# Kernel tuning notes

Measured on AMD Instinct MI355X. Metric: run time of the kernel, lower is better.

The kernel has to match this reference:

```python
import jax, jax.numpy as jnp
import numpy as np

LABEL_SMOOTH = 0.1

def setup_inputs() -> dict:
    key = jax.random.key(0)
    k1, k2, k3, k4 = jax.random.split(key, 4)
    B, S, D, V = 2, 2048, 1024, 50257
    targets = jax.random.randint(k1, (B, S), 0, V)              # int labels in [0, V)
    masks = jax.random.randint(k2, (B, S), 0, 2).astype(bool)   # valid-token mask
    outputs = jax.random.normal(k3, (B, S, D), dtype=jnp.float32)
    W = jax.random.normal(k4, (V, D), dtype=jnp.float32) * 0.02  # nn.Linear(d_model, V, bias=False).weight
    return {"targets": targets, "masks": masks, "outputs": outputs, "W": W}

def reference(targets, masks, outputs, W):
    # Faithful to IO.cost: gather masked tokens, project to vocab, label-smoothed NLL.
    # Boolean gather is expressed as mask-weighted means (identical math, jit-friendly).
    V = W.shape[0]
    logits = jnp.einsum('bsd,vd->bsv', outputs, W)        # [B,S,V] huge intermediate
    logp = jax.nn.log_softmax(logits, axis=-1)            # [B,S,V]
    m = masks.astype(logp.dtype)                          # [B,S]
    n_valid = m.sum()
    # F.nll_loss(logits, targets): mean of -logp[target] over valid tokens
    tok_logp = jnp.take_along_axis(logp, targets[..., None], axis=-1)[..., 0]  # [B,S]
    nll = -(m * tok_logp).sum() / n_valid
    # logits.mean(): mean of log-probs over valid tokens x vocab
    mean_logp = (m * logp.sum(axis=-1)).sum() / (n_valid * V)
    return nll * (1.0 - LABEL_SMOOTH) - mean_logp * LABEL_SMOOTH
```

## Files before the change

kernel.cpp:

```cpp
#include <hip/hip_runtime.h>
#include <hip/hip_bf16.h>
#include <stdint.h>

#define T_TOK 4096
#define DIM   1024
#define VOC   50257
#define VPAD  51200
#define BK    128
#define NKS   8

#define FRAGB  2048
#define PANB   16384

#define WSCALE 64.0f
#define INV_WSCALE 0.015625f

typedef __attribute__((ext_vector_type(8))) int  i32x8;
typedef __attribute__((ext_vector_type(4))) float f32x4;

__device__ __forceinline__ uint32_t pk4_fp8(float a, float b, float c, float d) {
  int u = 0;
  u = __builtin_amdgcn_cvt_pk_fp8_f32(a, b, u, false);
  u = __builtin_amdgcn_cvt_pk_fp8_f32(c, d, u, true);
  return (uint32_t)u;
}

__device__ __forceinline__ i32x8 ld32(const uint8_t* p) {
  const int4 lo = *(const int4*)p;
  const int4 hi = *(const int4*)(p + 16);
  i32x8 r;
  r[0] = lo.x; r[1] = lo.y; r[2] = lo.z; r[3] = lo.w;
  r[4] = hi.x; r[5] = hi.y; r[6] = hi.z; r[7] = hi.w;
  return r;
}

__global__ void k_scan(const int* __restrict__ masks, const int* __restrict__ targets,
                       int* __restrict__ hdr, int* __restrict__ cidx, int* __restrict__ tgtc,
                       float* __restrict__ Se, float* __restrict__ Sl) {
  __shared__ int cnt[256];
  const int tid = threadIdx.x;
  const int base = tid * 16;
  #pragma unroll
  for (int i = 0; i < 16; i++) { Se[base + i] = 0.f; Sl[base + i] = 0.f; }
  int c = 0;
  #pragma unroll
  for (int i = 0; i < 16; i++) c += (masks[base + i] != 0) ? 1 : 0;
  cnt[tid] = c;
  __syncthreads();
  for (int off = 1; off < 256; off <<= 1) {
    int add = (tid >= off) ? cnt[tid - off] : 0;
    __syncthreads();
    cnt[tid] += add;
    __syncthreads();
  }
  int start = cnt[tid] - c;
  for (int i = 0; i < 16; i++) {
    int t = base + i;
    if (masks[t] != 0) { cidx[start] = t; tgtc[start] = targets[t]; start++; }
  }
  if (tid == 255) hdr[0] = cnt[255];
}

__global__ void k_xconv(const float* __restrict__ X, const int* __restrict__ hdr,
                        const int* __restrict__ cidx, uint8_t* __restrict__ XqT) {
  const int c4 = blockIdx.x * 256 + threadIdx.x;
  const int slot = c4 >> 8;
  const int kq   = c4 & 255;
  const int p = slot >> 4, rlo = slot & 15;
  const int s = kq >> 5;
  const int w128 = kq & 31;
  const int q = w128 >> 3;
  const int b = (w128 & 7) * 4;
  const int l = q * 16 + rlo;
  const int nv = hdr[0];
  uint32_t o = 0;
  if (slot < nv) {
    const float4 v = *(const float4*)(X + (size_t)cidx[slot] * DIM + (size_t)kq * 4);
    o = pk4_fp8(v.x, v.y, v.z, v.w);
  }
  *(uint32_t*)(XqT + (size_t)(p * 8 + s) * 2048 + l * 32 + b) = o;
}

__global__ void k_wconv(const float* __restrict__ W, uint8_t* __restrict__ WqT) {
  const int c4 = blockIdx.x * 256 + threadIdx.x;
  const int row = c4 >> 8;
  const int kq  = c4 & 255;
  const int p = row >> 4, rlo = row & 15;
  const int s = kq >> 5;
  const int w128 = kq & 31;
  const int q = w128 >> 3;
  const int b = (w128 & 7) * 4;
  const int l = q * 16 + rlo;
  uint32_t o = 0;
  if (row < VOC) {
    const float4 v = *(const float4*)(W + (size_t)row * DIM + (size_t)kq * 4);
    o = pk4_fp8(v.x * WSCALE, v.y * WSCALE, v.z * WSCALE, v.w * WSCALE);
  }
  *(uint32_t*)(WqT + (size_t)(p * 8 + s) * 2048 + l * 32 + b) = o;
}

__global__ __launch_bounds__(256) void k_gemm(
    const uint8_t* __restrict__ XqT, const uint8_t* __restrict__ WqT,
    const int* __restrict__ hdr, const int* __restrict__ tgtc,
    float* __restrict__ tlog, float* __restrict__ Se, float* __restrict__ Sl) {
  const int flat = blockIdx.x;
  const int xcd = flat & 7;
  const int u = flat >> 3;
  const int ms = u & 63;
  const int ng = (u >> 6) * 8 + xcd;

  const int nv = hdr[0];
  const int m0 = ms * 64;
  if (m0 >= nv) return;

  const int tid = threadIdx.x;
  const int w    = tid >> 6;
  const int lane = tid & 63;
  const int quad = lane >> 4;
  const int l15  = lane & 15;
  const int n0w  = (ng * 4 + w) * 64;

  const uint8_t* pA[4];
  const uint8_t* pB[4];
  #pragma unroll
  for (int i = 0; i < 4; i++) {
    pA[i] = XqT + (size_t)(ms * 4 + i) * PANB + lane * 32;
    pB[i] = WqT + (size_t)((n0w >> 4) + i) * PANB + lane * 32;
  }

  f32x4 acc[4][4];
  #pragma unroll
  for (int i = 0; i < 4; i++)
    #pragma unroll
    for (int j = 0; j < 4; j++) { f32x4 z = {0.f, 0.f, 0.f, 0.f}; acc[i][j] = z; }

  const int sc1 = 0x7F7F7F7F;

  i32x8 a0[4], b0[4], a1[4], b1[4];
  #pragma unroll
  for (int i = 0; i < 4; i++) { a0[i] = ld32(pA[i]); b0[i] = ld32(pB[i]); }

  #pragma unroll
  for (int s = 0; s < NKS; s += 2) {
    if (s + 1 < NKS) {
      #pragma unroll
      for (int i = 0; i < 4; i++) {
        a1[i] = ld32(pA[i] + (s + 1) * FRAGB);
        b1[i] = ld32(pB[i] + (s + 1) * FRAGB);
      }
    }
    #pragma unroll
    for (int mi = 0; mi < 4; mi++)
      #pragma unroll
      for (int ni = 0; ni < 4; ni++)
        acc[mi][ni] = __builtin_amdgcn_mfma_scale_f32_16x16x128_f8f6f4(
            a0[mi], b0[ni], acc[mi][ni], 0, 0, 0, sc1, 0, sc1);
    if (s + 2 < NKS) {
      #pragma unroll
      for (int i = 0; i < 4; i++) {
        a0[i] = ld32(pA[i] + (s + 2) * FRAGB);
        b0[i] = ld32(pB[i] + (s + 2) * FRAGB);
      }
    }
    if (s + 1 < NKS) {
      #pragma unroll
      for (int mi = 0; mi < 4; mi++)
        #pragma unroll
        for (int ni = 0; ni < 4; ni++)
          acc[mi][ni] = __builtin_amdgcn_mfma_scale_f32_16x16x128_f8f6f4(
              a1[mi], b1[ni], acc[mi][ni], 0, 0, 0, sc1, 0, sc1);
    }
  }

  int tg[4][4];
  #pragma unroll
  for (int mi = 0; mi < 4; mi++) {
    const int4 t4 = *(const int4*)&tgtc[m0 + mi * 16 + quad * 4];
    tg[mi][0] = t4.x; tg[mi][1] = t4.y; tg[mi][2] = t4.z; tg[mi][3] = t4.w;
  }
  float rse[4][4], rsl[4][4];
  #pragma unroll
  for (int mi = 0; mi < 4; mi++)
    #pragma unroll
    for (int r = 0; r < 4; r++) { rse[mi][r] = 0.f; rsl[mi][r] = 0.f; }
  #pragma unroll
  for (int ni = 0; ni < 4; ni++) {
    const int v = n0w + ni * 16 + l15;
    if (v < VOC) {
      #pragma unroll
      for (int mi = 0; mi < 4; mi++)
        #pragma unroll
        for (int r = 0; r < 4; r++) {
          const float x = acc[mi][ni][r] * INV_WSCALE;
          rse[mi][r] += __expf(x);
          rsl[mi][r] += x;
          if (v == tg[mi][r]) tlog[m0 + mi * 16 + quad * 4 + r] = x;
        }
    }
  }
  #pragma unroll
  for (int off = 1; off < 16; off <<= 1)
    #pragma unroll
    for (int mi = 0; mi < 4; mi++)
      #pragma unroll
      for (int r = 0; r < 4; r++) {
        rse[mi][r] += __shfl_xor(rse[mi][r], off, 16);
        rsl[mi][r] += __shfl_xor(rsl[mi][r], off, 16);
      }

  __shared__ float seP[4][64], slP[4][64];
  if (l15 == 0) {
    #pragma unroll
    for (int mi = 0; mi < 4; mi++)
      #pragma unroll
      for (int r = 0; r < 4; r++) {
        const int row = mi * 16 + quad * 4 + r;
        seP[w][row] = rse[mi][r];
        slP[w][row] = rsl[mi][r];
      }
  }
  __syncthreads();
  if (tid < 64) {
    const int t = m0 + tid;
    if (t < nv) {
      atomicAdd(&Se[t], seP[0][tid] + seP[1][tid] + seP[2][tid] + seP[3][tid]);
      atomicAdd(&Sl[t], slP[0][tid] + slP[1][tid] + slP[2][tid] + slP[3][tid]);
    }
  }
}

__global__ void k_final(const int* __restrict__ hdr, const float* __restrict__ Se,
                        const float* __restrict__ Sl, const float* __restrict__ tlog,
                        float* __restrict__ out) {
  __shared__ float rn[256], rs[256];
  const int tid = threadIdx.x;
  const int nv = hdr[0];
  float nll = 0.f, slg = 0.f;
  for (int t = tid; t < nv; t += 256) {
    const float lse = logf(Se[t]);
    nll += lse - tlog[t];
    slg += Sl[t] - (float)VOC * lse;
  }
  rn[tid] = nll; rs[tid] = slg;
  __syncthreads();
  for (int off = 128; off > 0; off >>= 1) {
    if (tid < off) { rn[tid] += rn[tid + off]; rs[tid] += rs[tid + off]; }
    __syncthreads();
  }
  if (tid == 0) {
    const float fnv = (float)nv;
    out[0] = 0.9f * (rn[0] / fnv) - 0.1f * (rs[0] / (fnv * (float)VOC));
  }
}

extern "C" void kernel_launch(void* const* d_in, const int* in_sizes, int n_in,
                              void* d_out, int out_size, void* d_ws, size_t ws_size,
                              hipStream_t stream) {
  const int*   targets = (const int*)d_in[0];
  const int*   masks   = (const int*)d_in[1];
  const float* X       = (const float*)d_in[2];
  const float* W       = (const float*)d_in[3];

  uint8_t* ws = (uint8_t*)d_ws;
  size_t off = 0;
  auto alloc = [&](size_t n) { size_t p = off; off += (n + 255) & ~(size_t)255; return p; };
  int*      hdr  = (int*)     (ws + alloc(256));
  int*      cidx = (int*)     (ws + alloc((size_t)T_TOK * 4));
  int*      tgtc = (int*)     (ws + alloc((size_t)T_TOK * 4));
  float*    tlog = (float*)   (ws + alloc((size_t)T_TOK * 4));
  float*    Se   = (float*)   (ws + alloc((size_t)T_TOK * 4));
  float*    Sl   = (float*)   (ws + alloc((size_t)T_TOK * 4));
  uint8_t*  XqT  = (uint8_t*) (ws + alloc((size_t)T_TOK * DIM));
  uint8_t*  WqT  = (uint8_t*) (ws + alloc((size_t)VPAD * DIM));

  k_scan<<<dim3(1), dim3(256), 0, stream>>>(masks, targets, hdr, cidx, tgtc, Se, Sl);
  k_xconv<<<dim3(T_TOK * DIM / 4 / 256), dim3(256), 0, stream>>>(X, hdr, cidx, XqT);
  k_wconv<<<dim3(VPAD * DIM / 4 / 256), dim3(256), 0, stream>>>(W, WqT);
  k_gemm<<<dim3(64 * 200), dim3(256), 0, stream>>>(XqT, WqT, hdr, tgtc, tlog, Se, Sl);
  k_final<<<dim3(1), dim3(256), 0, stream>>>(hdr, Se, Sl, tlog, (float*)d_out);
}
```

Before: 591.6 us.

## Fuse W fp8 conversion into GEMM with LDS-resident vocab slice per block

Removes the separate W quantization kernel and its global round trip. Each GEMM block now loads a 64-row slice of W, converts it to fp8 into shared memory once, keeps the B fragments in registers, and loops over all token tiles streaming A from global. This cuts the 200MB fp32 W read plus fp8 write and re-read down to a single read. The cost is that only 786 blocks, each with a 64KB LDS tile, perform a serial loop over token tiles with syncs. Per-block compute is also reduced to 4 MFMAs per k-step, which may lower MFMA utilization and increase A-operand traffic.

```diff
diff --git a/kernel.cpp b/kernel.cpp
--- a/kernel.cpp
+++ b/kernel.cpp
@@ -5,8 +5,7 @@
 #define T_TOK 4096
 #define DIM   1024
 #define VOC   50257
-#define VPAD  51200
-#define BK    128
+#define NBLK  786
 #define NKS   8
 
 #define FRAGB  2048
@@ -81,151 +80,146 @@
   *(uint32_t*)(XqT + (size_t)(p * 8 + s) * 2048 + l * 32 + b) = o;
 }
 
-__global__ void k_wconv(const float* __restrict__ W, uint8_t* __restrict__ WqT) {
-  const int c4 = blockIdx.x * 256 + threadIdx.x;
-  const int row = c4 >> 8;
-  const int kq  = c4 & 255;
-  const int p = row >> 4, rlo = row & 15;
-  const int s = kq >> 5;
-  const int w128 = kq & 31;
-  const int q = w128 >> 3;
-  const int b = (w128 & 7) * 4;
-  const int l = q * 16 + rlo;
-  uint32_t o = 0;
-  if (row < VOC) {
-    const float4 v = *(const float4*)(W + (size_t)row * DIM + (size_t)kq * 4);
-    o = pk4_fp8(v.x * WSCALE, v.y * WSCALE, v.z * WSCALE, v.w * WSCALE);
-  }
-  *(uint32_t*)(WqT + (size_t)(p * 8 + s) * 2048 + l * 32 + b) = o;
-}
-
-__global__ __launch_bounds__(256) void k_gemm(
-    const uint8_t* __restrict__ XqT, const uint8_t* __restrict__ WqT,
+__global__ __launch_bounds__(256, 2) void k_gemm(
+    const uint8_t* __restrict__ XqT, const float* __restrict__ W,
     const int* __restrict__ hdr, const int* __restrict__ tgtc,
     float* __restrict__ tlog, float* __restrict__ Se, float* __restrict__ Sl) {
-  const int flat = blockIdx.x;
-  const int xcd = flat & 7;
-  const int u = flat >> 3;
-  const int ms = u & 63;
-  const int ng = (u >> 6) * 8 + xcd;
-
-  const int nv = hdr[0];
-  const int m0 = ms * 64;
-  if (m0 >= nv) return;
-
+  __shared__ __align__(16) uint8_t Blds[65536];
+  __shared__ float seP[4][64], slP[4][64];
+
+  const int bid = blockIdx.x;
+  const int v0  = bid * 64;
   const int tid = threadIdx.x;
   const int w    = tid >> 6;
   const int lane = tid & 63;
   const int quad = lane >> 4;
   const int l15  = lane & 15;
-  const int n0w  = (ng * 4 + w) * 64;
-
-  const uint8_t* pA[4];
-  const uint8_t* pB[4];
-  #pragma unroll
-  for (int i = 0; i < 4; i++) {
-    pA[i] = XqT + (size_t)(ms * 4 + i) * PANB + lane * 32;
-    pB[i] = WqT + (size_t)((n0w >> 4) + i) * PANB + lane * 32;
-  }
-
-  f32x4 acc[4][4];
-  #pragma unroll
-  for (int i = 0; i < 4; i++)
-    #pragma unroll
-    for (int j = 0; j < 4; j++) { f32x4 z = {0.f, 0.f, 0.f, 0.f}; acc[i][j] = z; }
+
+  const int nv = hdr[0];
+  const int mloops = (nv + 63) >> 6;
+
+  {
+    const int s    = tid >> 5;
+    const int half = (tid & 4) ? 1024 : 0;
+    const int sub  = (tid >> 3) & 3;
+    const int b4   = (tid & 3) * 4;
+    #pragma unroll 8
+    for (int r = 0; r < 64; r++) {
+      const int row = v0 + r;
+      uint32_t o = 0;
+      if (row < VOC) {
+        const float4 v = *(const float4*)(W + (size_t)row * DIM + (size_t)tid * 4);
+        o = pk4_fp8(v.x * WSCALE, v.y * WSCALE, v.z * WSCALE, v.w * WSCALE);
+      }
+      const int fb = (r >> 4) * 8 + s;
+      const int l  = sub * 16 + (r & 15);
+      *(uint32_t*)(Blds + fb * 2048 + half + l * 16 + b4) = o;
+    }
+  }
+  __syncthreads();
+
+  i32x8 bf[8];
+  #pragma unroll
+  for (int s = 0; s < 8; s++) {
+    const uint8_t* p = Blds + (w * 8 + s) * 2048 + lane * 16;
+    const int4 lo = *(const int4*)p;
+    const int4 hi = *(const int4*)(p + 1024);
+    bf[s][0] = lo.x; bf[s][1] = lo.y; bf[s][2] = lo.z; bf[s][3] = lo.w;
+    bf[s][4] = hi.x; bf[s][5] = hi.y; bf[s][6] = hi.z; bf[s][7] = hi.w;
+  }
 
   const int sc1 = 0x7F7F7F7F;
-
-  i32x8 a0[4], b0[4], a1[4], b1[4];
-  #pragma unroll
-  for (int i = 0; i < 4; i++) { a0[i] = ld32(pA[i]); b0[i] = ld32(pB[i]); }
-
-  #pragma unroll
-  for (int s = 0; s < NKS; s += 2) {
-    if (s + 1 < NKS) {
-      #pragma unroll
-      for (int i = 0; i < 4; i++) {
-        a1[i] = ld32(pA[i] + (s + 1) * FRAGB);
-        b1[i] = ld32(pB[i] + (s + 1) * FRAGB);
+  const uint8_t* pA = XqT + lane * 32;
+  const int vcol = v0 + w * 16 + l15;
+
+  i32x8 a0[4], a1[4];
+  #pragma unroll
+  for (int i = 0; i < 4; i++) a0[i] = ld32(pA + (size_t)i * PANB);
+
+  for (int mt = 0; mt < mloops; mt++) {
+    const int m0 = mt * 64;
+    const size_t mb = (size_t)mt * 4 * PANB;
+
+    f32x4 acc[4];
+    #pragma unroll
+    for (int i = 0; i < 4; i++) { f32x4 z = {0.f, 0.f, 0.f, 0.f}; acc[i] = z; }
+
+    #pragma unroll
+    for (int s = 0; s < NKS; s += 2) {
+      #pragma unroll
+      for (int i = 0; i < 4; i++)
+        a1[i] = ld32(pA + mb + (size_t)i * PANB + (s + 1) * FRAGB);
+      #pragma unroll
+      for (int mi = 0; mi < 4; mi++)
+        acc[mi] = __builtin_amdgcn_mfma_scale_f32_16x16x128_f8f6f4(
+            a0[mi], bf[s], acc[mi], 0, 0, 0, sc1, 0, sc1);
+      if (s + 2 < NKS) {
+        #pragma unroll
+        for (int i = 0; i < 4; i++)
+          a0[i] = ld32(pA + mb + (size_t)i * PANB + (s + 2) * FRAGB);
       }
-    }
+      #pragma unroll
+      for (int mi = 0; mi < 4; mi++)
+        acc[mi] = __builtin_amdgcn_mfma_scale_f32_16x16x128_f8f6f4(
+            a1[mi], bf[s + 1], acc[mi], 0, 0, 0, sc1, 0, sc1);
+    }
+
+    if (mt + 1 < mloops) {
+      #pragma unroll
+      for (int i = 0; i < 4; i++)
+        a0[i] = ld32(pA + (size_t)(mt + 1) * 4 * PANB + (size_t)i * PANB);
+    }
+
+    int tg[4][4];
+    #pragma unroll
+    for (int mi = 0; mi < 4; mi++) {
+      const int4 t4 = *(const int4*)&tgtc[m0 + mi * 16 + quad * 4];
+      tg[mi][0] = t4.x; tg[mi][1] = t4.y; tg[mi][2] = t4.z; tg[mi][3] = t4.w;
+    }
+    float rse[4][4], rsl[4][4];
     #pragma unroll
     for (int mi = 0; mi < 4; mi++)
       #pragma unroll
-      for (int ni = 0; ni < 4; ni++)
-        acc[mi][ni] = __builtin_amdgcn_mfma_scale_f32_16x16x128_f8f6f4(
-            a0[mi], b0[ni], acc[mi][ni], 0, 0, 0, sc1, 0, sc1);
-    if (s + 2 < NKS) {
-      #pragma unroll
-      for (int i = 0; i < 4; i++) {
-        a0[i] = ld32(pA[i] + (s + 2) * FRAGB);
-        b0[i] = ld32(pB[i] + (s + 2) * FRAGB);
-      }
-    }
-    if (s + 1 < NKS) {
-      #pragma unroll
-      for (int mi = 0; mi < 4; mi++)
-        #pragma unroll
-        for (int ni = 0; ni < 4; ni++)
-          acc[mi][ni] = __builtin_amdgcn_mfma_scale_f32_16x16x128_f8f6f4(
-              a1[mi], b1[ni], acc[mi][ni], 0, 0, 0, sc1, 0, sc1);
-    }
-  }
-
-  int tg[4][4];
-  #pragma unroll
-  for (int mi = 0; mi < 4; mi++) {
-    const int4 t4 = *(const int4*)&tgtc[m0 + mi * 16 + quad * 4];
-    tg[mi][0] = t4.x; tg[mi][1] = t4.y; tg[mi][2] = t4.z; tg[mi][3] = t4.w;
-  }
-  float rse[4][4], rsl[4][4];
-  #pragma unroll
-  for (int mi = 0; mi < 4; mi++)
-    #pragma unroll
-    for (int r = 0; r < 4; r++) { rse[mi][r] = 0.f; rsl[mi][r] = 0.f; }
-  #pragma unroll
-  for (int ni = 0; ni < 4; ni++) {
-    const int v = n0w + ni * 16 + l15;
-    if (v < VOC) {
+      for (int r = 0; r < 4; r++) { rse[mi][r] = 0.f; rsl[mi][r] = 0.f; }
+    if (vcol < VOC) {
       #pragma unroll
       for (int mi = 0; mi < 4; mi++)
         #pragma unroll
         for (int r = 0; r < 4; r++) {
-          const float x = acc[mi][ni][r] * INV_WSCALE;
+          const float x = acc[mi][r] * INV_WSCALE;
           rse[mi][r] += __expf(x);
           rsl[mi][r] += x;
-          if (v == tg[mi][r]) tlog[m0 + mi * 16 + quad * 4 + r] = x;
+          if (vcol == tg[mi][r]) tlog[m0 + mi * 16 + quad * 4 + r] = x;
         }
     }
-  }
-  #pragma unroll
-  for (int off = 1; off < 16; off <<= 1)
-    #pragma unroll
-    for (int mi = 0; mi < 4; mi++)
-      #pragma unroll
-      for (int r = 0; r < 4; r++) {
-        rse[mi][r] += __shfl_xor(rse[mi][r], off, 16);
-        rsl[mi][r] += __shfl_xor(rsl[mi][r], off, 16);
+    #pragma unroll
+    for (int off = 1; off < 16; off <<= 1)
+      #pragma unroll
+      for (int mi = 0; mi < 4; mi++)
+        #pragma unroll
+        for (int r = 0; r < 4; r++) {
+          rse[mi][r] += __shfl_xor(rse[mi][r], off, 16);
+          rsl[mi][r] += __shfl_xor(rsl[mi][r], off, 16);
+        }
+    if (l15 == 0) {
+      #pragma unroll
+      for (int mi = 0; mi < 4; mi++)
+        #pragma unroll
+        for (int r = 0; r < 4; r++) {
+          const int row = mi * 16 + quad * 4 + r;
+          seP[w][row] = rse[mi][r];
+          slP[w][row] = rsl[mi][r];
+        }
+    }
+    __syncthreads();
+    if (tid < 64) {
+      const int t = m0 + tid;
+      if (t < nv) {
+        atomicAdd(&Se[t], seP[0][tid] + seP[1][tid] + seP[2][tid] + seP[3][tid]);
+        atomicAdd(&Sl[t], slP[0][tid] + slP[1][tid] + slP[2][tid] + slP[3][tid]);
       }
-
-  __shared__ float seP[4][64], slP[4][64];
-  if (l15 == 0) {
-    #pragma unroll
-    for (int mi = 0; mi < 4; mi++)
-      #pragma unroll
-      for (int r = 0; r < 4; r++) {
-        const int row = mi * 16 + quad * 4 + r;
-        seP[w][row] = rse[mi][r];
-        slP[w][row] = rsl[mi][r];
-      }
-  }
-  __syncthreads();
-  if (tid < 64) {
-    const int t = m0 + tid;
-    if (t < nv) {
-      atomicAdd(&Se[t], seP[0][tid] + seP[1][tid] + seP[2][tid] + seP[3][tid]);
-      atomicAdd(&Sl[t], slP[0][tid] + slP[1][tid] + slP[2][tid] + slP[3][tid]);
-    }
+    }
+    __syncthreads();
   }
 }
 
@@ -271,11 +265,9 @@
   float*    Se   = (float*)   (ws + alloc((size_t)T_TOK * 4));
   float*    Sl   = (float*)   (ws + alloc((size_t)T_TOK * 4));
   uint8_t*  XqT  = (uint8_t*) (ws + alloc((size_t)T_TOK * DIM));
-  uint8_t*  WqT  = (uint8_t*) (ws + alloc((size_t)VPAD * DIM));
 
   k_scan<<<dim3(1), dim3(256), 0, stream>>>(masks, targets, hdr, cidx, tgtc, Se, Sl);
   k_xconv<<<dim3(T_TOK * DIM / 4 / 256), dim3(256), 0, stream>>>(X, hdr, cidx, XqT);
-  k_wconv<<<dim3(VPAD * DIM / 4 / 256), dim3(256), 0, stream>>>(W, WqT);
-  k_gemm<<<dim3(64 * 200), dim3(256), 0, stream>>>(XqT, WqT, hdr, tgtc, tlog, Se, Sl);
+  k_gemm<<<dim3(NBLK), dim3(256), 0, stream>>>(XqT, W, hdr, tgtc, tlog, Se, Sl);
   k_final<<<dim3(1), dim3(256), 0, stream>>>(hdr, Se, Sl, tlog, (float*)d_out);
 }
```

Result: slower. 1.953 ms (+230.1%).
